# Kernel optimization log

Hardware: AMD Instinct MI355X
Metric: run time of the kernel (lower is better)

The kernel has to match this reference:

```python
import jax, jax.numpy as jnp
import numpy as np


def _cd2(a, b):
    # squared euclidean distances [n,m]
    d = jnp.sum(a * a, 1)[:, None] + jnp.sum(b * b, 1)[None, :] - 2.0 * (a @ b.T)
    return jnp.maximum(d, 0.0)


def _cdist(a, b):
    # tiny clamp keeps sqrt grad finite on the zero diagonal, fwd unchanged
    return jnp.sqrt(jnp.maximum(_cd2(a, b), 1e-30))


def _tmedian(x):
    # torch.median semantics: lower middle element
    f = jnp.sort(x.reshape(-1))
    return f[(f.shape[0] - 1) // 2]


def setup_inputs() -> dict:
    key = jax.random.key(0)
    k1, k2 = jax.random.split(key)
    feat_s = jax.random.normal(k1, (25, 640), dtype=jnp.float32)
    y_s = (jnp.arange(25) % 5).astype(jnp.int32)  # 5-way 5-shot, every class present
    feat_q = jax.random.normal(k2, (300, 640), dtype=jnp.float32)
    return {"feat_s": feat_s, "y_s": y_s, "feat_q": feat_q}


def reference(feat_s, y_s, feat_q):
    y_s_np = np.asarray(y_s)
    classes = np.unique(y_s_np)
    C = int(classes.shape[0])
    onehot = jnp.asarray(y_s_np[:, None] == classes[None, :], dtype=feat_s.dtype)  # [S,C]
    prototypes = (onehot.T @ feat_s) / jnp.sum(onehot, 0)[:, None]  # [C,D]

    # ---- virtual mixup densification ----
    dist_q = _cdist(feat_q, prototypes)  # [Nq,C]
    y_boot = np.asarray(jnp.argmin(dist_q, 1))
    q_norm = feat_q / jnp.linalg.norm(feat_q, axis=1, keepdims=True)
    cos_np = np.asarray(q_norm @ q_norm.T)
    dist_q_np = np.asarray(dist_q)
    virt = []
    for c in range(C):
        idx = np.flatnonzero(y_boot == c)
        if idx.size < 2:
            continue
        cos_c = cos_np[np.ix_(idx, idx)]
        f = np.sort(cos_c.reshape(-1))
        thresh = f[(f.size - 1) // 2]  # torch lower median
        ii, jj = np.nonzero(np.triu(cos_c >= thresh, 1))  # pairs with i<j
        if ii.size:
            virt.append(0.5 * (feat_q[idx[ii]] + feat_q[idx[jj]]))
        kq = int(idx[np.argmin(dist_q_np[idx, c])])
        virt.append((0.5 * (prototypes[c] + feat_q[kq]))[None, :])
    feat_all = jnp.concatenate([feat_q] + virt, 0) if virt else feat_q

    # ---- self-tuning affinity (kNN graph) ----
    n = int(feat_all.shape[0])
    k = max(1, int(np.log2(n)))
    dist = _cdist(feat_all, feat_all)  # [n,n]
    _, nn_idx = jax.lax.top_k(-dist, k + 1)  # smallest k+1 (incl. self)
    sigma = dist[jnp.arange(n), nn_idx[:, k]] + 1e-8
    nbrs = nn_idx[:, 1:]  # [n,k]
    d_nb = jnp.take_along_axis(dist, nbrs, 1)
    w = jnp.exp(-d_nb / (sigma[:, None] * sigma[nbrs]))
    W = jnp.zeros((n, n), feat_all.dtype).at[jnp.arange(n)[:, None], nbrs].set(w)
    W = (W + W.T) / 2
    D_inv = 1.0 / (W.sum(1) + 1e-8)

    # ---- density-adaptive lambda ----
    d = _cdist(feat_all, prototypes).min(1)
    lam = jnp.exp(-(d ** 2) / (2 * _tmedian(d) ** 2 + 1e-8))

    # ---- mm iterations (label propagation) ----
    a = _cd2(feat_all, prototypes)  # [n,C]
    y0 = jax.nn.softmax(-a, axis=1)
    scale = (lam * D_inv)[:, None]

    def step(carry, _):
        y, done = carry
        y_new = jax.nn.softmax(-a + scale * (W @ y), axis=1)
        conv = jnp.max(jnp.abs(y_new - y)) < 1e-4
        y_out = jnp.where(done | conv, y, y_new)  # emulate torch early break
        return (y_out, done | conv), None

    (y, _), _ = jax.lax.scan(step, (y0, jnp.asarray(False)), None, length=50)
    preds = jnp.argmax(y[: feat_q.shape[0]], 1)
    return preds
```

## Files before the change

### kernel.cpp

```cpp
#include <hip/hip_runtime.h>
#include <math.h>

#define CMAX 8
#define KMAX 16
#define TPB 256
#define BNMAX 512

struct P {
  const float* fs; const int* ys; const float* fq;
  int S, Q, D, BN, NMAX;
  float* proto;
  float* G;
  float* cosq;
  int* ybt;
  int* cls; int* scount; int* qcount; int* qidx; int* kq;
  float* thr;
  int* rowcnt; int* rowoff; int* paircnt; int* basev;
  int* meta;
  int* uv;
  float* rn2;
  int* nbrs; float* dnb; float* wgt; float* sigma;
  int* indeg; int* inoff; int* cursor;
  int* insrcU; float* inwU; int* indst;
  int* insrc; float* inw;
  unsigned* cosk;
  unsigned* gmaxu;
  float* amat; float* dinv; float* dmin; float* scalev;
  float* yA; float* yB;
  float* meddenom;
  int* outp;
};

__device__ inline unsigned f2key(float f){
  unsigned b=__float_as_uint(f);
  return (b&0x80000000u)? ~b : (b|0x80000000u);
}
__device__ inline float key2f(unsigned k){
  unsigned b=(k&0x80000000u)? (k^0x80000000u) : ~k;
  return __uint_as_float(b);
}
__device__ inline unsigned long long shfl_xor_u64(unsigned long long v,int m){
  unsigned lo=(unsigned)v, hi=(unsigned)(v>>32);
  lo=__shfl_xor(lo,m,64); hi=__shfl_xor(hi,m,64);
  return (((unsigned long long)hi)<<32)|lo;
}

__global__ void k_init(P p){
  if (threadIdx.x==0){
    int labs[CMAX]; int cnt[CMAX]; int C=0;
    for (int s=0;s<p.S;s++){
      int l=p.ys[s]; int f=-1;
      for(int c=0;c<C;c++) if(labs[c]==l){f=c;break;}
      if(f<0){ if(C<CMAX){labs[C]=l;cnt[C]=1;C++;} }
      else cnt[f]++;
    }
    for(int a=0;a<C;a++)for(int b=a+1;b<C;b++)
      if(labs[b]<labs[a]){int t=labs[a];labs[a]=labs[b];labs[b]=t;
                          t=cnt[a];cnt[a]=cnt[b];cnt[b]=t;}
    for(int c=0;c<C;c++){p.cls[c]=labs[c];p.scount[c]=cnt[c];}
    p.meta[0]=C;
  }
}

__global__ void k_proto(P p){
  int c=blockIdx.x; int C=p.meta[0];
  for(int d=threadIdx.x; d<p.D; d+=blockDim.x){
    float s=0.f;
    if(c<C){
      int lab=p.cls[c];
      for(int j=0;j<p.S;j++) if(p.ys[j]==lab) s+=p.fs[(size_t)j*p.D+d];
      s/= (float)p.scount[c];
    }
    p.proto[(size_t)c*p.D+d]=s;
  }
}

__global__ void k_gram(P p){
  __shared__ float arow[1024];
  int a=blockIdx.x;
  const float* ra = (a<p.Q)? p.fq + (size_t)a*p.D : p.proto + (size_t)(a-p.Q)*p.D;
  const float* A = ra;
  if(p.D<=1024){
    for(int d=threadIdx.x; d<p.D; d+=blockDim.x) arow[d]=ra[d];
    __syncthreads();
    A=(const float*)arow;
  }
  int D4=p.D>>2; int Dt=D4<<2;
  for(int b=threadIdx.x; b<p.BN; b+=blockDim.x){
    const float* rb=(b<p.Q)? p.fq+(size_t)b*p.D : p.proto+(size_t)(b-p.Q)*p.D;
    const float4* a4=(const float4*)A;
    const float4* b4=(const float4*)rb;
    float s=0.f;
    #pragma unroll 4
    for(int d=0;d<D4;d++){
      float4 x=a4[d], y=b4[d];
      s += x.x*y.x + x.y*y.y + x.z*y.z + x.w*y.w;
    }
    for(int d=Dt;d<p.D;d++) s += A[d]*rb[d];
    p.G[(size_t)a*p.BN+b]=s;
  }
}

__global__ void k_cos(P p){
  int t=blockIdx.x*blockDim.x+threadIdx.x;
  if(t>=p.Q*p.Q)return;
  int i=t/p.Q, j=t%p.Q;
  p.cosq[t]=p.G[(size_t)i*p.BN+j]/(sqrtf(p.G[(size_t)i*p.BN+i])*sqrtf(p.G[(size_t)j*p.BN+j]));
}

__global__ void k_yboot(P p){
  int q=blockIdx.x*blockDim.x+threadIdx.x;
  if(q>=p.Q)return;
  int C=p.meta[0];
  float gq=p.G[(size_t)q*p.BN+q];
  float best=INFINITY; int bc=0;
  for(int c=0;c<C;c++){
    int pc=p.Q+c;
    float d2=gq+p.G[(size_t)pc*p.BN+pc]-2.f*p.G[(size_t)q*p.BN+pc];
    d2=fmaxf(d2,0.f);
    if(d2<best){best=d2;bc=c;}
  }
  p.ybt[q]=bc;
}

__global__ void k_qidx(P p){
  int c=blockIdx.x; int C=p.meta[0];
  int lane=threadIdx.x;
  if(c>=C){ if(lane==0){p.qcount[c]=0;p.kq[c]=0;} return; }
  int base=0;
  for(int q0=0;q0<p.Q;q0+=64){
    int q=q0+lane;
    bool in = (q<p.Q) && (p.ybt[q]==c);
    unsigned long long mask=__ballot(in);
    int pre=__popcll(mask & ((lane==63)?0x7FFFFFFFFFFFFFFFull:((1ull<<lane)-1ull)));
    if(in) p.qidx[c*p.Q+base+pre]=q;
    base+=__popcll(mask);
  }
  if(lane==0) p.qcount[c]=base;
  int pc=p.Q+c;
  float gp=p.G[(size_t)pc*p.BN+pc];
  unsigned long long best=0xFFFFFFFFFFFFFFFFull;
  for(int t=lane;t<base;t+=64){
    int q=p.qidx[c*p.Q+t];
    float d2=fmaxf(p.G[(size_t)q*p.BN+q]+gp-2.f*p.G[(size_t)q*p.BN+pc],0.f);
    unsigned long long key=(((unsigned long long)f2key(d2))<<32)|(unsigned)t;
    if(key<best)best=key;
  }
  #pragma unroll
  for(int s=32;s>=1;s>>=1){
    unsigned long long o=shfl_xor_u64(best,s);
    if(o<best)best=o;
  }
  if(lane==0){
    int t=(int)(unsigned)(best&0xFFFFFFFFull);
    p.kq[c]=(base>0)? p.qidx[c*p.Q+t] : 0;
  }
}

__global__ void k_median(P p){
  __shared__ unsigned hist[256];
  __shared__ unsigned sPref; __shared__ int sTrem;
  __shared__ int sqidx[512];
  int c=blockIdx.x; int C=p.meta[0];
  int m=(c<C)? p.qcount[c]:0;
  int tid=threadIdx.x;
  if(m<2){ if(tid==0) p.thr[c]=INFINITY; return; }
  const int* qix;
  if(p.Q<=512){
    for(int t=tid;t<m;t+=blockDim.x) sqidx[t]=p.qidx[c*p.Q+t];
    __syncthreads();
    qix=sqidx;
  } else qix=p.qidx+c*p.Q;
  int total=m*m;
  unsigned* keys=p.cosk+(size_t)c*p.Q*p.Q;
  for(int t=tid;t<total;t+=blockDim.x){
    int a=t/m, b=t-a*m;
    keys[t]=f2key(p.cosq[(size_t)qix[a]*p.Q+qix[b]]);
  }
  if(tid==0){ sPref=0u; sTrem=(total-1)/2; }
  __syncthreads();
  unsigned prefmask=0u;
  for(int shift=24;shift>=0;shift-=8){
    hist[tid&255]=0u;
    __syncthreads();
    unsigned pref=sPref;
    for(int t=tid;t<total;t+=blockDim.x){
      unsigned key=keys[t];
      if((key&prefmask)==pref) atomicAdd(&hist[(key>>shift)&255],1u);
    }
    __syncthreads();
    if(tid==0){
      int trem=sTrem; unsigned cum=0;
      for(int b=0;b<256;b++){
        unsigned h=hist[b];
        if(cum+h>(unsigned)trem){ sPref=pref|((unsigned)b<<shift); sTrem=trem-(int)cum; break; }
        cum+=h;
      }
    }
    __syncthreads();
    prefmask|=(0xFFu<<shift);
  }
  if(tid==0) p.thr[c]=key2f(sPref);
}

__global__ void k_rowcnt(P p){
  int c=blockIdx.x; int C=p.meta[0];
  int m=(c<C)? p.qcount[c]:0;
  if(m<2){ if(threadIdx.x==0) p.paircnt[c]=0; return; }
  float th=p.thr[c];
  for(int a=threadIdx.x;a<m;a+=blockDim.x){
    int ia=p.qidx[c*p.Q+a]; int cnt=0;
    const float* row=p.cosq+(size_t)ia*p.Q;
    for(int b=a+1;b<m;b++){
      int ib=p.qidx[c*p.Q+b];
      cnt += (row[ib]>=th);
    }
    p.rowcnt[c*p.Q+a]=cnt;
  }
  __syncthreads();
  if(threadIdx.x==0){
    int run=0;
    for(int a=0;a<m;a++){p.rowoff[c*p.Q+a]=run; run+=p.rowcnt[c*p.Q+a];}
    p.paircnt[c]=run;
  }
}

__global__ void k_bases(P p){
  int C=p.meta[0]; int cur=p.Q;
  for(int c=0;c<C;c++){
    p.basev[c]=cur;
    if(p.qcount[c]>=2) cur += p.paircnt[c]+1;
  }
  int n=cur; if(n>p.NMAX)n=p.NMAX;
  p.meta[1]=n;
  int k=31-__clz(n); if(k<1)k=1; if(k>KMAX-1)k=KMAX-1;
  p.meta[2]=k;
  p.meta[3]=0;
  p.meta[4]=0;
  p.meta[5]=0;
  for(int t=0;t<64;t++) p.gmaxu[t]=0u;
}

__global__ void k_uv(P p){
  int r=blockIdx.x*blockDim.x+threadIdx.x;
  if(r>=p.NMAX)return;
  p.indeg[r]=0;
  if(r<p.Q){ p.uv[2*r]=r; p.uv[2*r+1]=r; }
}

__global__ void k_uvpairs(P p){
  int c=blockIdx.x; int C=p.meta[0];
  int m=(c<C)? p.qcount[c]:0;
  if(m<2)return;
  float th=p.thr[c];
  int bs=p.basev[c];
  for(int a=threadIdx.x;a<m;a+=blockDim.x){
    int ia=p.qidx[c*p.Q+a];
    int off=bs+p.rowoff[c*p.Q+a]; int cnt=0;
    const float* row=p.cosq+(size_t)ia*p.Q;
    for(int b=a+1;b<m;b++){
      int ib=p.qidx[c*p.Q+b];
      if(row[ib]>=th){
        int r=off+cnt;
        p.uv[2*r]=ia; p.uv[2*r+1]=ib;
        cnt++;
      }
    }
  }
  if(threadIdx.x==0){
    int r=bs+p.paircnt[c];
    p.uv[2*r]=p.Q+c; p.uv[2*r+1]=p.kq[c];
  }
}

__global__ void k_rn2(P p){
  int r=blockIdx.x*blockDim.x+threadIdx.x;
  int n=p.meta[1]; if(r>=n)return;
  int u=p.uv[2*r],v=p.uv[2*r+1];
  p.rn2[r]=0.25f*(p.G[(size_t)u*p.BN+u]+2.f*p.G[(size_t)u*p.BN+v]+p.G[(size_t)v*p.BN+v]);
}

__global__ void k_knn(P p){
  __shared__ float sGu[BNMAX];
  __shared__ float sGv[BNMAX];
  int i=blockIdx.x;
  int n=p.meta[1]; if(i>=n)return;
  int kp1=p.meta[2]+1;
  int lane=threadIdx.x;
  int u1=p.uv[2*i], v1=p.uv[2*i+1];
  const float* Gu=p.G+(size_t)u1*p.BN;
  const float* Gv=p.G+(size_t)v1*p.BN;
  const float* bu=Gu; const float* bv=Gv;
  if(p.BN<=BNMAX){
    for(int d=lane; d<p.BN; d+=64){ sGu[d]=Gu[d]; sGv[d]=Gv[d]; }
    __syncthreads();
    bu=(const float*)sGu; bv=(const float*)sGv;
  }
  float rni=p.rn2[i];
  unsigned long long r[16];
  #pragma unroll
  for(int t=0;t<16;t++) r[t]=0xFFFFFFFFFFFFFFFFull;
  for(int j=lane;j<n;j+=64){
    int2 w=((const int2*)p.uv)[j];
    float dot=0.25f*(bu[w.x]+bu[w.y]+bv[w.x]+bv[w.y]);
    float d2=fmaxf(rni+p.rn2[j]-2.f*dot,0.f);
    unsigned long long key=(((unsigned long long)f2key(d2))<<32)|(unsigned)j;
    if(key<r[15]){
      #pragma unroll
      for(int t=0;t<16;t++){
        unsigned long long lo=key<r[t]?key:r[t];
        unsigned long long hi=key<r[t]?r[t]:key;
        r[t]=lo; key=hi;
      }
    }
  }
  for(int t=0;t<kp1;t++){
    unsigned long long m=r[0];
    #pragma unroll
    for(int s=32;s>=1;s>>=1){
      unsigned long long o=shfl_xor_u64(m,s);
      if(o<m)m=o;
    }
    if(r[0]==m){
      #pragma unroll
      for(int q=0;q<15;q++) r[q]=r[q+1];
      r[15]=0xFFFFFFFFFFFFFFFFull;
    }
    if(lane==0){
      int j=(int)(unsigned)(m&0xFFFFFFFFull);
      float d2=key2f((unsigned)(m>>32));
      float dd=sqrtf(fmaxf(d2,1e-30f));
      if(t>=1){ p.nbrs[(size_t)i*KMAX+t-1]=j; p.dnb[(size_t)i*KMAX+t-1]=dd; }
      if(t==kp1-1) p.sigma[i]=dd+1e-8f;
    }
  }
}

__global__ void k_wgtcnt(P p){
  int i=blockIdx.x*blockDim.x+threadIdx.x;
  int n=p.meta[1]; if(i>=n)return;
  int k=p.meta[2];
  float si=p.sigma[i];
  for(int q=0;q<k;q++){
    int j=p.nbrs[(size_t)i*KMAX+q];
    p.wgt[(size_t)i*KMAX+q]=expf(-p.dnb[(size_t)i*KMAX+q]/(si*p.sigma[j]));
    atomicAdd(&p.indeg[j],1);
  }
}

__global__ void k_scan(P p){
  __shared__ int part[TPB];
  int n=p.meta[1];
  int chunk=(n+TPB-1)/TPB;
  int beg=threadIdx.x*chunk, end=beg+chunk; if(end>n)end=n;
  int s=0;
  for(int i=beg;i<end;i++) s+=p.indeg[i];
  part[threadIdx.x]=s; __syncthreads();
  if(threadIdx.x==0){
    int run=0;
    for(int t=0;t<TPB;t++){int v=part[t];part[t]=run;run+=v;}
    p.inoff[n]=run;
  }
  __syncthreads();
  int run=part[threadIdx.x];
  for(int i=beg;i<end;i++){
    p.inoff[i]=run; p.cursor[i]=run; run+=p.indeg[i];
  }
}

__global__ void k_fill(P p){
  int i=blockIdx.x*blockDim.x+threadIdx.x;
  int n=p.meta[1]; if(i>=n)return;
  int k=p.meta[2];
  for(int q=0;q<k;q++){
    int dst=p.nbrs[(size_t)i*KMAX+q];
    int slot=atomicAdd(&p.cursor[dst],1);
    p.insrcU[slot]=i; p.inwU[slot]=p.wgt[(size_t)i*KMAX+q]; p.indst[slot]=dst;
  }
}

__global__ void k_rank(P p){
  int e=blockIdx.x*blockDim.x+threadIdx.x;
  int n=p.meta[1];
  int E=p.inoff[n];
  if(e>=E)return;
  int dst=p.indst[e];
  int b=p.inoff[dst], en=p.inoff[dst+1];
  int s=p.insrcU[e]; float w=p.inwU[e];
  int rank=0;
  for(int x=b;x<en;x++) rank += (p.insrcU[x]<s);
  p.insrc[b+rank]=s; p.inw[b+rank]=w;
}

__global__ void k_dad(P p){
  int i=blockIdx.x*blockDim.x+threadIdx.x;
  int n=p.meta[1]; if(i>=n)return;
  int k=p.meta[2]; int C=p.meta[0];
  float s=0.f;
  for(int q=0;q<k;q++) s+=p.wgt[(size_t)i*KMAX+q];
  for(int e=p.inoff[i];e<p.inoff[i+1];e++) s+=p.inw[e];
  p.dinv[i]=1.f/(0.5f*s+1e-8f);
  int u=p.uv[2*i],v=p.uv[2*i+1];
  float rn=p.rn2[i]; float mn=INFINITY;
  #pragma unroll
  for(int c=0;c<CMAX;c++){
    float a=INFINITY;
    if(c<C){
      int pc=p.Q+c;
      a=rn+p.G[(size_t)pc*p.BN+pc]-(p.G[(size_t)u*p.BN+pc]+p.G[(size_t)v*p.BN+pc]);
      a=fmaxf(a,0.f);
      mn=fminf(mn,a);
    }
    p.amat[(size_t)i*CMAX+c]=a;
  }
  p.dmin[i]=sqrtf(fmaxf(mn,1e-30f));
}

__global__ void k_medd(P p){
  __shared__ unsigned hist[256];
  __shared__ unsigned sPref; __shared__ int sTrem;
  int n=p.meta[1];
  int tid=threadIdx.x;
  if(tid==0){ sPref=0u; sTrem=(n-1)/2; }
  __syncthreads();
  unsigned prefmask=0u;
  for(int shift=24;shift>=0;shift-=8){
    hist[tid&255]=0u;
    __syncthreads();
    unsigned pref=sPref;
    for(int i=tid;i<n;i+=blockDim.x){
      unsigned key=f2key(p.dmin[i]);
      if((key&prefmask)==pref) atomicAdd(&hist[(key>>shift)&255],1u);
    }
    __syncthreads();
    if(tid==0){
      int trem=sTrem; unsigned cum=0;
      for(int b=0;b<256;b++){
        unsigned h=hist[b];
        if(cum+h>(unsigned)trem){ sPref=pref|((unsigned)b<<shift); sTrem=trem-(int)cum; break; }
        cum+=h;
      }
    }
    __syncthreads();
    prefmask|=(0xFFu<<shift);
  }
  if(tid==0){
    float med=key2f(sPref);
    p.meddenom[0]=2.f*med*med+1e-8f;
  }
}

__global__ void k_y0(P p){
  int i=blockIdx.x*blockDim.x+threadIdx.x;
  int n=p.meta[1]; if(i>=n)return;
  float la=expf(-(p.dmin[i]*p.dmin[i])/p.meddenom[0]);
  p.scalev[i]=la*p.dinv[i];
  float mn=INFINITY;
  #pragma unroll
  for(int c=0;c<CMAX;c++) mn=fminf(mn,p.amat[(size_t)i*CMAX+c]);
  float ex[CMAX]; float sum=0.f;
  #pragma unroll
  for(int c=0;c<CMAX;c++){
    float e=expf(mn-p.amat[(size_t)i*CMAX+c]);
    ex[c]=e; sum+=e;
  }
  float inv=1.f/sum;
  #pragma unroll
  for(int c=0;c<CMAX;c++) p.yA[(size_t)i*CMAX+c]=ex[c]*inv;
}

__global__ void k_step(P p,int t){
  if(p.meta[3]) return;
  int n=p.meta[1]; int k=p.meta[2];
  int par=p.meta[4];
  float* cur=par? p.yB : p.yA;
  float* nxt=par? p.yA : p.yB;
  int i=blockIdx.x*blockDim.x+threadIdx.x;
  float dmx=0.f;
  if(i<n){
    float4 wa=make_float4(0.f,0.f,0.f,0.f), wb=make_float4(0.f,0.f,0.f,0.f);
    #pragma unroll 4
    for(int q=0;q<k;q++){
      int j=p.nbrs[(size_t)i*KMAX+q];
      float w=p.wgt[(size_t)i*KMAX+q];
      const float4* yr=(const float4*)(cur+(size_t)j*CMAX);
      float4 y0=yr[0],y1=yr[1];
      wa.x+=w*y0.x; wa.y+=w*y0.y; wa.z+=w*y0.z; wa.w+=w*y0.w;
      wb.x+=w*y1.x; wb.y+=w*y1.y; wb.z+=w*y1.z; wb.w+=w*y1.w;
    }
    int e1=p.inoff[i+1];
    for(int e=p.inoff[i];e<e1;e++){
      int j=p.insrc[e]; float w=p.inw[e];
      const float4* yr=(const float4*)(cur+(size_t)j*CMAX);
      float4 y0=yr[0],y1=yr[1];
      wa.x+=w*y0.x; wa.y+=w*y0.y; wa.z+=w*y0.z; wa.w+=w*y0.w;
      wb.x+=w*y1.x; wb.y+=w*y1.y; wb.z+=w*y1.z; wb.w+=w*y1.w;
    }
    float sc=p.scalev[i]*0.5f;
    const float4* am=(const float4*)(p.amat+(size_t)i*CMAX);
    float4 a0=am[0],a1=am[1];
    float l0=sc*wa.x-a0.x, l1=sc*wa.y-a0.y, l2=sc*wa.z-a0.z, l3=sc*wa.w-a0.w;
    float l4=sc*wb.x-a1.x, l5=sc*wb.y-a1.y, l6=sc*wb.z-a1.z, l7=sc*wb.w-a1.w;
    float mx=fmaxf(fmaxf(fmaxf(l0,l1),fmaxf(l2,l3)),fmaxf(fmaxf(l4,l5),fmaxf(l6,l7)));
    float e0=expf(l0-mx),e1f=expf(l1-mx),e2=expf(l2-mx),e3=expf(l3-mx);
    float e4=expf(l4-mx),e5=expf(l5-mx),e6=expf(l6-mx),e7=expf(l7-mx);
    float inv=1.f/(e0+e1f+e2+e3+e4+e5+e6+e7);
    float4 o0=make_float4(e0*inv,e1f*inv,e2*inv,e3*inv);
    float4 o1=make_float4(e4*inv,e5*inv,e6*inv,e7*inv);
    const float4* cr=(const float4*)(cur+(size_t)i*CMAX);
    float4 c0=cr[0],c1=cr[1];
    dmx=fmaxf(dmx,fabsf(o0.x-c0.x)); dmx=fmaxf(dmx,fabsf(o0.y-c0.y));
    dmx=fmaxf(dmx,fabsf(o0.z-c0.z)); dmx=fmaxf(dmx,fabsf(o0.w-c0.w));
    dmx=fmaxf(dmx,fabsf(o1.x-c1.x)); dmx=fmaxf(dmx,fabsf(o1.y-c1.y));
    dmx=fmaxf(dmx,fabsf(o1.z-c1.z)); dmx=fmaxf(dmx,fabsf(o1.w-c1.w));
    float4* nr=(float4*)(nxt+(size_t)i*CMAX);
    nr[0]=o0; nr[1]=o1;
  }
  #pragma unroll
  for(int s=32;s>=1;s>>=1) dmx=fmaxf(dmx,__shfl_xor(dmx,s,64));
  if(threadIdx.x==0){
    atomicMax(p.gmaxu+t,__float_as_uint(dmx));
    __threadfence();
    int fin=atomicAdd(&p.meta[5],1);
    if(fin==(int)gridDim.x-1){
      p.meta[5]=0;
      float mm=__uint_as_float(p.gmaxu[t]);
      if(mm<1e-4f) p.meta[3]=1;
      else         p.meta[4]=par^1;
    }
  }
}

__global__ void k_arg(P p){
  int q=blockIdx.x*blockDim.x+threadIdx.x;
  if(q>=p.Q)return;
  int C=p.meta[0];
  const float* cur=p.meta[4]? p.yB : p.yA;
  float best=cur[(size_t)q*CMAX+0]; int bc=0;
  for(int c=1;c<C;c++){
    float v=cur[(size_t)q*CMAX+c];
    if(v>best){best=v;bc=c;}
  }
  p.outp[q]=bc;
}


static void make_layout(char* base,int S,int Q,int D,int BN,long N,
                        const float*fs,const int*ys,const float*fq,
                        int* outp, P* pp, size_t* need){
  size_t off=0;
  auto A=[&](size_t b)->char*{
    size_t o=(off+255)&~(size_t)255; off=o+b; return base+o;
  };
  P p{};
  p.fs=fs;p.ys=ys;p.fq=fq;p.S=S;p.Q=Q;p.D=D;p.BN=BN;p.NMAX=(int)N;
  p.proto=(float*)A(4ul*CMAX*D);
  p.G=(float*)A(4ul*(size_t)BN*BN);
  p.cosq=(float*)A(4ul*(size_t)Q*Q);
  p.ybt=(int*)A(4ul*Q);
  p.cls=(int*)A(4ul*CMAX);
  p.scount=(int*)A(4ul*CMAX);
  p.qcount=(int*)A(4ul*CMAX);
  p.qidx=(int*)A(4ul*CMAX*Q);
  p.kq=(int*)A(4ul*CMAX);
  p.thr=(float*)A(4ul*CMAX);
  p.rowcnt=(int*)A(4ul*CMAX*Q);
  p.rowoff=(int*)A(4ul*CMAX*Q);
  p.paircnt=(int*)A(4ul*CMAX);
  p.basev=(int*)A(4ul*CMAX);
  p.meta=(int*)A(4ul*16);
  p.uv=(int*)A(8ul*N);
  p.rn2=(float*)A(4ul*N);
  p.nbrs=(int*)A(4ul*KMAX*N);
  p.dnb=(float*)A(4ul*KMAX*N);
  p.wgt=(float*)A(4ul*KMAX*N);
  p.sigma=(float*)A(4ul*N);
  p.indeg=(int*)A(4ul*N);
  p.inoff=(int*)A(4ul*(N+1));
  p.cursor=(int*)A(4ul*N);
  p.insrcU=(int*)A(4ul*KMAX*N);
  p.inwU=(float*)A(4ul*KMAX*N);
  p.indst=(int*)A(4ul*KMAX*N);
  p.insrc=(int*)A(4ul*KMAX*N);
  p.inw=(float*)A(4ul*KMAX*N);
  p.cosk=(unsigned*)A(4ul*CMAX*(size_t)Q*Q);
  p.gmaxu=(unsigned*)A(4ul*64);
  p.amat=(float*)A(4ul*CMAX*N);
  p.dinv=(float*)A(4ul*N);
  p.dmin=(float*)A(4ul*N);
  p.scalev=(float*)A(4ul*N);
  p.yA=(float*)A(4ul*CMAX*N);
  p.yB=(float*)A(4ul*CMAX*N);
  p.meddenom=(float*)A(4ul*4);
  p.outp=outp;
  *pp=p; *need=off;
}

extern "C" void kernel_launch(void* const* d_in, const int* in_sizes, int n_in,
                              void* d_out, int out_size, void* d_ws, size_t ws_size,
                              hipStream_t stream){
  const float* fs=(const float*)d_in[0];
  const int*   ys=(const int*)d_in[1];
  const float* fq=(const float*)d_in[2];
  int S=in_sizes[1];
  int D=in_sizes[0]/S;
  int Q=in_sizes[2]/D;
  int BN=Q+CMAX;

  long full=(long)Q + (long)Q*(Q-1)/2 + CMAX;
  long cand[4]={full,16384,8192,5000};
  P p{}; size_t need=0; int NMAX=(int)cand[3];
  for(int ci=0;ci<4;ci++){
    long N=cand[ci]; if(N<Q+CMAX)N=Q+CMAX;
    make_layout((char*)d_ws,S,Q,D,BN,N,fs,ys,fq,(int*)d_out,&p,&need);
    NMAX=(int)N;
    if(need<=ws_size) break;
  }

  int gN=(NMAX+TPB-1)/TPB;
  long gEl=((long)NMAX*KMAX+TPB-1)/TPB;
  int gE=(int)gEl;
  int gS=(NMAX+63)/64;

  k_init   <<<1, 64, 0, stream>>>(p);
  k_proto  <<<CMAX, TPB, 0, stream>>>(p);
  k_gram   <<<BN, TPB, 0, stream>>>(p);
  k_cos    <<<(Q*Q+TPB-1)/TPB, TPB, 0, stream>>>(p);
  k_yboot  <<<(Q+TPB-1)/TPB, TPB, 0, stream>>>(p);
  k_qidx   <<<CMAX, 64, 0, stream>>>(p);
  k_median <<<CMAX, TPB, 0, stream>>>(p);
  k_rowcnt <<<CMAX, TPB, 0, stream>>>(p);
  k_bases  <<<1, 1, 0, stream>>>(p);
  k_uv     <<<gN, TPB, 0, stream>>>(p);
  k_uvpairs<<<CMAX, TPB, 0, stream>>>(p);
  k_rn2    <<<gN, TPB, 0, stream>>>(p);
  k_knn    <<<NMAX, 64, 0, stream>>>(p);
  k_wgtcnt <<<gN, TPB, 0, stream>>>(p);
  k_scan   <<<1, TPB, 0, stream>>>(p);
  k_fill   <<<gN, TPB, 0, stream>>>(p);
  k_rank   <<<gE, TPB, 0, stream>>>(p);
  k_dad    <<<gN, TPB, 0, stream>>>(p);
  k_medd   <<<1, TPB, 0, stream>>>(p);
  k_y0     <<<gN, TPB, 0, stream>>>(p);
  for(int t=0;t<50;t++)
    k_step <<<gS, 64, 0, stream>>>(p, t);
  k_arg    <<<(Q+TPB-1)/TPB, TPB, 0, stream>>>(p);
}
```

Before: 611.5 us.

## Fuse label-propagation iterations into one persistent kernel and precompute kNN rows

Replaces the 50 per-iteration k_step launches plus k_y0 and k_arg with a single persistent kernel. It uses a software grid barrier, keeps neighbor indices and weights in registers, and exits early on convergence. The kNN stage now precomputes a per-row half-sum of Gram rows (H) and a packed candidate array, so each distance needs two shared loads instead of four. It also adds a templated smaller selection buffer and a periodic wave-wide threshold to prune insertions. The cost is extra memory for H and a spin-barrier that relies on all blocks being co-resident.

After: 738.5 us. 20.8% more time.

```diff
diff --git a/kernel.cpp b/kernel.cpp
--- a/kernel.cpp
+++ b/kernel.cpp
@@ -4,7 +4,7 @@
 #define CMAX 8
 #define KMAX 16
 #define TPB 256
-#define BNMAX 512
+#define BNMAX 1024
 
 struct P {
   const float* fs; const int* ys; const float* fq;
@@ -19,6 +19,8 @@
   int* meta;
   int* uv;
   float* rn2;
+  float* H;
+  int* cand;
   int* nbrs; float* dnb; float* wgt; float* sigma;
   int* indeg; int* inoff; int* cursor;
   int* insrcU; float* inwU; int* indst;
@@ -235,9 +237,9 @@
   p.meta[1]=n;
   int k=31-__clz(n); if(k<1)k=1; if(k>KMAX-1)k=KMAX-1;
   p.meta[2]=k;
-  p.meta[3]=0;
-  p.meta[4]=0;
+  p.meta[3]=0; p.meta[4]=0;
   p.meta[5]=0;
+  p.meta[6]=0;
   for(int t=0;t<64;t++) p.gmaxu[t]=0u;
 }
 
@@ -273,45 +275,56 @@
   }
 }
 
-__global__ void k_rn2(P p){
-  int r=blockIdx.x*blockDim.x+threadIdx.x;
-  int n=p.meta[1]; if(r>=n)return;
-  int u=p.uv[2*r],v=p.uv[2*r+1];
-  p.rn2[r]=0.25f*(p.G[(size_t)u*p.BN+u]+2.f*p.G[(size_t)u*p.BN+v]+p.G[(size_t)v*p.BN+v]);
-}
-
-__global__ void k_knn(P p){
-  __shared__ float sGu[BNMAX];
-  __shared__ float sGv[BNMAX];
+__global__ void k_hrow(P p){
   int i=blockIdx.x;
   int n=p.meta[1]; if(i>=n)return;
-  int kp1=p.meta[2]+1;
+  int u=p.uv[2*i], v=p.uv[2*i+1];
+  const float* Gu=p.G+(size_t)u*p.BN;
+  const float* Gv=p.G+(size_t)v*p.BN;
+  float* h=p.H+(size_t)i*p.BN;
+  for(int x=threadIdx.x;x<p.BN;x+=64) h[x]=0.5f*(Gu[x]+Gv[x]);
+  __syncthreads();
+  if(threadIdx.x==0){
+    float rn=0.5f*(h[u]+h[v]);
+    p.rn2[i]=rn;
+    ((int4*)p.cand)[i]=make_int4(u,v,__float_as_int(rn),0);
+  }
+}
+
+template<int KSEL>
+__device__ void knn_body(const P& p,int i,int n,int kp1,const float* sh,float rni){
   int lane=threadIdx.x;
-  int u1=p.uv[2*i], v1=p.uv[2*i+1];
-  const float* Gu=p.G+(size_t)u1*p.BN;
-  const float* Gv=p.G+(size_t)v1*p.BN;
-  const float* bu=Gu; const float* bv=Gv;
-  if(p.BN<=BNMAX){
-    for(int d=lane; d<p.BN; d+=64){ sGu[d]=Gu[d]; sGv[d]=Gv[d]; }
-    __syncthreads();
-    bu=(const float*)sGu; bv=(const float*)sGv;
-  }
-  float rni=p.rn2[i];
-  unsigned long long r[16];
+  unsigned long long r[KSEL];
   #pragma unroll
-  for(int t=0;t<16;t++) r[t]=0xFFFFFFFFFFFFFFFFull;
-  for(int j=lane;j<n;j+=64){
-    int2 w=((const int2*)p.uv)[j];
-    float dot=0.25f*(bu[w.x]+bu[w.y]+bv[w.x]+bv[w.y]);
-    float d2=fmaxf(rni+p.rn2[j]-2.f*dot,0.f);
-    unsigned long long key=(((unsigned long long)f2key(d2))<<32)|(unsigned)j;
-    if(key<r[15]){
+  for(int t=0;t<KSEL;t++) r[t]=0xFFFFFFFFFFFFFFFFull;
+  unsigned long long thrw=0xFFFFFFFFFFFFFFFFull;
+  int iters=(n+63)>>6;
+  const int4* cand=(const int4*)p.cand;
+  for(int it=0;it<iters;++it){
+    int j=(it<<6)+lane;
+    unsigned long long key=0xFFFFFFFFFFFFFFFFull;
+    if(j<n){
+      int4 cd=cand[j];
+      float d2=fmaxf(rni+__int_as_float(cd.z)-sh[cd.x]-sh[cd.y],0.f);
+      key=(((unsigned long long)f2key(d2))<<32)|(unsigned)j;
+    }
+    if(key<thrw && key<r[KSEL-1]){
       #pragma unroll
-      for(int t=0;t<16;t++){
-        unsigned long long lo=key<r[t]?key:r[t];
-        unsigned long long hi=key<r[t]?r[t]:key;
+      for(int t=0;t<KSEL;t++){
+        bool lt=key<r[t];
+        unsigned long long lo=lt?key:r[t];
+        unsigned long long hi=lt?r[t]:key;
         r[t]=lo; key=hi;
       }
+    }
+    if((it&15)==15){
+      unsigned long long v=r[KSEL-1];
+      #pragma unroll
+      for(int s=32;s>=1;s>>=1){
+        unsigned long long o=shfl_xor_u64(v,s);
+        if(o<v)v=o;
+      }
+      thrw=v;
     }
   }
   for(int t=0;t<kp1;t++){
@@ -323,8 +336,8 @@
     }
     if(r[0]==m){
       #pragma unroll
-      for(int q=0;q<15;q++) r[q]=r[q+1];
-      r[15]=0xFFFFFFFFFFFFFFFFull;
+      for(int q=0;q<KSEL-1;q++) r[q]=r[q+1];
+      r[KSEL-1]=0xFFFFFFFFFFFFFFFFull;
     }
     if(lane==0){
       int j=(int)(unsigned)(m&0xFFFFFFFFull);
@@ -334,6 +347,23 @@
       if(t==kp1-1) p.sigma[i]=dd+1e-8f;
     }
   }
+}
+
+__global__ void k_knn(P p){
+  __shared__ float sh[BNMAX];
+  int i=blockIdx.x;
+  int n=p.meta[1]; if(i>=n)return;
+  int kp1=p.meta[2]+1;
+  const float* h=p.H+(size_t)i*p.BN;
+  const float* hp=h;
+  if(p.BN<=BNMAX){
+    for(int d=threadIdx.x;d<p.BN;d+=64) sh[d]=h[d];
+    __syncthreads();
+    hp=(const float*)sh;
+  }
+  float rni=p.rn2[i];
+  if(kp1<=13) knn_body<13>(p,i,n,kp1,hp,rni);
+  else        knn_body<16>(p,i,n,kp1,hp,rni);
 }
 
 __global__ void k_wgtcnt(P p){
@@ -346,6 +376,7 @@
     p.wgt[(size_t)i*KMAX+q]=expf(-p.dnb[(size_t)i*KMAX+q]/(si*p.sigma[j]));
     atomicAdd(&p.indeg[j],1);
   }
+  for(int q=k;q<KMAX;q++){ p.nbrs[(size_t)i*KMAX+q]=i; p.wgt[(size_t)i*KMAX+q]=0.f; }
 }
 
 __global__ void k_scan(P p){
@@ -450,98 +481,108 @@
   }
 }
 
-__global__ void k_y0(P p){
-  int i=blockIdx.x*blockDim.x+threadIdx.x;
-  int n=p.meta[1]; if(i>=n)return;
-  float la=expf(-(p.dmin[i]*p.dmin[i])/p.meddenom[0]);
-  p.scalev[i]=la*p.dinv[i];
-  float mn=INFINITY;
-  #pragma unroll
-  for(int c=0;c<CMAX;c++) mn=fminf(mn,p.amat[(size_t)i*CMAX+c]);
-  float ex[CMAX]; float sum=0.f;
-  #pragma unroll
-  for(int c=0;c<CMAX;c++){
-    float e=expf(mn-p.amat[(size_t)i*CMAX+c]);
-    ex[c]=e; sum+=e;
-  }
-  float inv=1.f/sum;
-  #pragma unroll
-  for(int c=0;c<CMAX;c++) p.yA[(size_t)i*CMAX+c]=ex[c]*inv;
-}
-
-__global__ void k_step(P p,int t){
-  if(p.meta[3]) return;
-  int n=p.meta[1]; int k=p.meta[2];
-  int par=p.meta[4];
-  float* cur=par? p.yB : p.yA;
-  float* nxt=par? p.yA : p.yB;
-  int i=blockIdx.x*blockDim.x+threadIdx.x;
-  float dmx=0.f;
+__device__ inline void gridbar(int* cnt,int* gen,int nblk){
+  __syncthreads();
+  if(threadIdx.x==0){
+    __threadfence();
+    int g=atomicAdd(gen,0);
+    if(atomicAdd(cnt,1)==nblk-1){
+      atomicExch(cnt,0);
+      __threadfence();
+      atomicAdd(gen,1);
+    } else {
+      while(atomicAdd(gen,0)==g){ __builtin_amdgcn_s_sleep(16); }
+    }
+    __threadfence();
+  }
+  __syncthreads();
+}
+
+__global__ void __launch_bounds__(64) k_prop(P p){
+  int n=p.meta[1]; int C=p.meta[0];
+  int nblk=(int)gridDim.x;
+  int* cnt=p.meta+5; int* gen=p.meta+6;
+  int i=blockIdx.x*64+threadIdx.x;
+  int lane=threadIdx.x;
+
+  float sc=0.f; float4 a0=make_float4(0,0,0,0), a1=a0;
+  int nb[KMAX]; float wv[KMAX];
+  int e0=0,e1=0;
   if(i<n){
-    float4 wa=make_float4(0.f,0.f,0.f,0.f), wb=make_float4(0.f,0.f,0.f,0.f);
-    #pragma unroll 4
-    for(int q=0;q<k;q++){
-      int j=p.nbrs[(size_t)i*KMAX+q];
-      float w=p.wgt[(size_t)i*KMAX+q];
-      const float4* yr=(const float4*)(cur+(size_t)j*CMAX);
-      float4 y0=yr[0],y1=yr[1];
-      wa.x+=w*y0.x; wa.y+=w*y0.y; wa.z+=w*y0.z; wa.w+=w*y0.w;
-      wb.x+=w*y1.x; wb.y+=w*y1.y; wb.z+=w*y1.z; wb.w+=w*y1.w;
-    }
-    int e1=p.inoff[i+1];
-    for(int e=p.inoff[i];e<e1;e++){
-      int j=p.insrc[e]; float w=p.inw[e];
-      const float4* yr=(const float4*)(cur+(size_t)j*CMAX);
-      float4 y0=yr[0],y1=yr[1];
-      wa.x+=w*y0.x; wa.y+=w*y0.y; wa.z+=w*y0.z; wa.w+=w*y0.w;
-      wb.x+=w*y1.x; wb.y+=w*y1.y; wb.z+=w*y1.z; wb.w+=w*y1.w;
-    }
-    float sc=p.scalev[i]*0.5f;
     const float4* am=(const float4*)(p.amat+(size_t)i*CMAX);
-    float4 a0=am[0],a1=am[1];
-    float l0=sc*wa.x-a0.x, l1=sc*wa.y-a0.y, l2=sc*wa.z-a0.z, l3=sc*wa.w-a0.w;
-    float l4=sc*wb.x-a1.x, l5=sc*wb.y-a1.y, l6=sc*wb.z-a1.z, l7=sc*wb.w-a1.w;
-    float mx=fmaxf(fmaxf(fmaxf(l0,l1),fmaxf(l2,l3)),fmaxf(fmaxf(l4,l5),fmaxf(l6,l7)));
-    float e0=expf(l0-mx),e1f=expf(l1-mx),e2=expf(l2-mx),e3=expf(l3-mx);
-    float e4=expf(l4-mx),e5=expf(l5-mx),e6=expf(l6-mx),e7=expf(l7-mx);
-    float inv=1.f/(e0+e1f+e2+e3+e4+e5+e6+e7);
-    float4 o0=make_float4(e0*inv,e1f*inv,e2*inv,e3*inv);
-    float4 o1=make_float4(e4*inv,e5*inv,e6*inv,e7*inv);
-    const float4* cr=(const float4*)(cur+(size_t)i*CMAX);
-    float4 c0=cr[0],c1=cr[1];
-    dmx=fmaxf(dmx,fabsf(o0.x-c0.x)); dmx=fmaxf(dmx,fabsf(o0.y-c0.y));
-    dmx=fmaxf(dmx,fabsf(o0.z-c0.z)); dmx=fmaxf(dmx,fabsf(o0.w-c0.w));
-    dmx=fmaxf(dmx,fabsf(o1.x-c1.x)); dmx=fmaxf(dmx,fabsf(o1.y-c1.y));
-    dmx=fmaxf(dmx,fabsf(o1.z-c1.z)); dmx=fmaxf(dmx,fabsf(o1.w-c1.w));
-    float4* nr=(float4*)(nxt+(size_t)i*CMAX);
-    nr[0]=o0; nr[1]=o1;
-  }
-  #pragma unroll
-  for(int s=32;s>=1;s>>=1) dmx=fmaxf(dmx,__shfl_xor(dmx,s,64));
-  if(threadIdx.x==0){
-    atomicMax(p.gmaxu+t,__float_as_uint(dmx));
-    __threadfence();
-    int fin=atomicAdd(&p.meta[5],1);
-    if(fin==(int)gridDim.x-1){
-      p.meta[5]=0;
-      float mm=__uint_as_float(p.gmaxu[t]);
-      if(mm<1e-4f) p.meta[3]=1;
-      else         p.meta[4]=par^1;
-    }
-  }
-}
-
-__global__ void k_arg(P p){
-  int q=blockIdx.x*blockDim.x+threadIdx.x;
-  if(q>=p.Q)return;
-  int C=p.meta[0];
-  const float* cur=p.meta[4]? p.yB : p.yA;
-  float best=cur[(size_t)q*CMAX+0]; int bc=0;
-  for(int c=1;c<C;c++){
-    float v=cur[(size_t)q*CMAX+c];
-    if(v>best){best=v;bc=c;}
-  }
-  p.outp[q]=bc;
+    a0=am[0]; a1=am[1];
+    float la=expf(-(p.dmin[i]*p.dmin[i])/p.meddenom[0]);
+    sc=la*p.dinv[i]*0.5f;
+    float mn=fminf(fminf(fminf(a0.x,a0.y),fminf(a0.z,a0.w)),
+                   fminf(fminf(a1.x,a1.y),fminf(a1.z,a1.w)));
+    float e0f=expf(mn-a0.x),e1f=expf(mn-a0.y),e2f=expf(mn-a0.z),e3f=expf(mn-a0.w);
+    float e4f=expf(mn-a1.x),e5f=expf(mn-a1.y),e6f=expf(mn-a1.z),e7f=expf(mn-a1.w);
+    float inv=1.f/(e0f+e1f+e2f+e3f+e4f+e5f+e6f+e7f);
+    float4* y=(float4*)(p.yA+(size_t)i*CMAX);
+    y[0]=make_float4(e0f*inv,e1f*inv,e2f*inv,e3f*inv);
+    y[1]=make_float4(e4f*inv,e5f*inv,e6f*inv,e7f*inv);
+    #pragma unroll
+    for(int q=0;q<KMAX;q++){ nb[q]=p.nbrs[(size_t)i*KMAX+q]; wv[q]=p.wgt[(size_t)i*KMAX+q]; }
+    e0=p.inoff[i]; e1=p.inoff[i+1];
+  } else {
+    #pragma unroll
+    for(int q=0;q<KMAX;q++){ nb[q]=0; wv[q]=0.f; }
+  }
+  gridbar(cnt,gen,nblk);
+
+  float* cur=p.yA; float* nxt=p.yB;
+  for(int t=0;t<50;t++){
+    float dmx=0.f;
+    if(i<n){
+      float wax=0,way=0,waz=0,waw=0,wbx=0,wby=0,wbz=0,wbw=0;
+      #pragma unroll
+      for(int q=0;q<KMAX;q++){
+        const float4* yr=(const float4*)(cur+(size_t)nb[q]*CMAX);
+        float4 y0=yr[0],y1=yr[1];
+        float w=wv[q];
+        wax+=w*y0.x; way+=w*y0.y; waz+=w*y0.z; waw+=w*y0.w;
+        wbx+=w*y1.x; wby+=w*y1.y; wbz+=w*y1.z; wbw+=w*y1.w;
+      }
+      for(int e=e0;e<e1;e++){
+        int j=p.insrc[e]; float w=p.inw[e];
+        const float4* yr=(const float4*)(cur+(size_t)j*CMAX);
+        float4 y0=yr[0],y1=yr[1];
+        wax+=w*y0.x; way+=w*y0.y; waz+=w*y0.z; waw+=w*y0.w;
+        wbx+=w*y1.x; wby+=w*y1.y; wbz+=w*y1.z; wbw+=w*y1.w;
+      }
+      float l0=sc*wax-a0.x, l1=sc*way-a0.y, l2=sc*waz-a0.z, l3=sc*waw-a0.w;
+      float l4=sc*wbx-a1.x, l5=sc*wby-a1.y, l6=sc*wbz-a1.z, l7=sc*wbw-a1.w;
+      float mx=fmaxf(fmaxf(fmaxf(l0,l1),fmaxf(l2,l3)),fmaxf(fmaxf(l4,l5),fmaxf(l6,l7)));
+      float x0=expf(l0-mx),x1=expf(l1-mx),x2=expf(l2-mx),x3=expf(l3-mx);
+      float x4=expf(l4-mx),x5=expf(l5-mx),x6=expf(l6-mx),x7=expf(l7-mx);
+      float inv=1.f/(x0+x1+x2+x3+x4+x5+x6+x7);
+      float4 o0=make_float4(x0*inv,x1*inv,x2*inv,x3*inv);
+      float4 o1=make_float4(x4*inv,x5*inv,x6*inv,x7*inv);
+      const float4* cr=(const float4*)(cur+(size_t)i*CMAX);
+      float4 c0=cr[0],c1=cr[1];
+      dmx=fmaxf(dmx,fabsf(o0.x-c0.x)); dmx=fmaxf(dmx,fabsf(o0.y-c0.y));
+      dmx=fmaxf(dmx,fabsf(o0.z-c0.z)); dmx=fmaxf(dmx,fabsf(o0.w-c0.w));
+      dmx=fmaxf(dmx,fabsf(o1.x-c1.x)); dmx=fmaxf(dmx,fabsf(o1.y-c1.y));
+      dmx=fmaxf(dmx,fabsf(o1.z-c1.z)); dmx=fmaxf(dmx,fabsf(o1.w-c1.w));
+      float4* nr=(float4*)(nxt+(size_t)i*CMAX);
+      nr[0]=o0; nr[1]=o1;
+    }
+    #pragma unroll
+    for(int s=32;s>=1;s>>=1) dmx=fmaxf(dmx,__shfl_xor(dmx,s,64));
+    if(lane==0) atomicMax(p.gmaxu+t,__float_as_uint(dmx));
+    gridbar(cnt,gen,nblk);
+    float mm=__uint_as_float(atomicAdd(p.gmaxu+t,0u));
+    if(mm<1e-4f) break;
+    float* tmp=cur;cur=nxt;nxt=tmp;
+  }
+  if(i<p.Q){
+    float best=cur[(size_t)i*CMAX+0]; int bc=0;
+    for(int c=1;c<C;c++){
+      float v=cur[(size_t)i*CMAX+c];
+      if(v>best){best=v;bc=c;}
+    }
+    p.outp[i]=bc;
+  }
 }
 
 
@@ -571,6 +612,8 @@
   p.meta=(int*)A(4ul*16);
   p.uv=(int*)A(8ul*N);
   p.rn2=(float*)A(4ul*N);
+  p.H=(float*)A(4ul*(size_t)N*BN);
+  p.cand=(int*)A(16ul*N);
   p.nbrs=(int*)A(4ul*KMAX*N);
   p.dnb=(float*)A(4ul*KMAX*N);
   p.wgt=(float*)A(4ul*KMAX*N);
@@ -633,7 +676,7 @@
   k_bases  <<<1, 1, 0, stream>>>(p);
   k_uv     <<<gN, TPB, 0, stream>>>(p);
   k_uvpairs<<<CMAX, TPB, 0, stream>>>(p);
-  k_rn2    <<<gN, TPB, 0, stream>>>(p);
+  k_hrow   <<<NMAX, 64, 0, stream>>>(p);
   k_knn    <<<NMAX, 64, 0, stream>>>(p);
   k_wgtcnt <<<gN, TPB, 0, stream>>>(p);
   k_scan   <<<1, TPB, 0, stream>>>(p);
@@ -641,8 +684,5 @@
   k_rank   <<<gE, TPB, 0, stream>>>(p);
   k_dad    <<<gN, TPB, 0, stream>>>(p);
   k_medd   <<<1, TPB, 0, stream>>>(p);
-  k_y0     <<<gN, TPB, 0, stream>>>(p);
-  for(int t=0;t<50;t++)
-    k_step <<<gS, 64, 0, stream>>>(p, t);
-  k_arg    <<<(Q+TPB-1)/TPB, TPB, 0, stream>>>(p);
-}
+  k_prop   <<<gS, 64, 0, stream>>>(p);
+}
```
